# Kernel optimization log

Measured on AMD Instinct MI355X. Metric: run time of the kernel, lower is better.

Reference implementation:

```python
import jax, jax.numpy as jnp
import numpy as np

N, K, C = 2, 512, 256
IMG = 1024.0
P = 7            # output_size
S = 2            # sampling_ratio
SCALES = (0.25, 0.125, 0.0625, 0.03125)
MIN_LEVEL, MAX_LEVEL = 2, 5
CANON_SIZE, CANON_LEVEL = 224.0, 4


def setup_inputs() -> dict:
    key = jax.random.key(0)
    ks = jax.random.split(key, 7)
    feats = {}
    for i, (hw, kk) in enumerate(zip((256, 128, 64, 32), ks[:4])):
        feats[f"feat{i + 2}"] = jax.random.normal(kk, (N, C, hw, hw), dtype=jnp.float32)
    # boxes: centers uniform in image, sizes log-uniform in [32, 512] px -> spans all levels
    cxy = jax.random.uniform(ks[4], (N, K, 2), minval=0.0, maxval=IMG)
    wh = 32.0 * jnp.exp2(jax.random.uniform(ks[5], (N, K, 2), minval=0.0, maxval=4.0))
    x1y1 = jnp.clip(cxy - wh / 2, 0.0, IMG)
    x2y2 = jnp.clip(cxy + wh / 2, 0.0, IMG)
    boxes = jnp.concatenate([x1y1, x2y2], axis=-1).astype(jnp.float32)  # [N,K,4] xyxy
    feats["boxes"] = boxes
    return feats


def _roi_align_level(feat, boxes, batch_idx, scale):
    """ROIAlignV2 (aligned=True). feat [N,C,H,W], boxes [M,4] xyxy in image coords."""
    Nf, Cf, H, W = feat.shape
    M = boxes.shape[0]
    b = boxes * scale - 0.5  # aligned=True shift
    x1, y1, x2, y2 = b[:, 0], b[:, 1], b[:, 2], b[:, 3]
    bin_h = (y2 - y1) / P
    bin_w = (x2 - x1) / P
    # combined bin+sample grid: coord = start + ((i + 0.5)/S) * bin, i in [0, P*S)
    g = (jnp.arange(P * S, dtype=feat.dtype) + 0.5) / S  # [PS]
    y = y1[:, None] + g[None, :] * bin_h[:, None]  # [M, PS]
    x = x1[:, None] + g[None, :] * bin_w[:, None]  # [M, PS]

    def prep(c, size):
        valid = (c >= -1.0) & (c <= size)
        c = jnp.maximum(c, 0.0)
        lo = jnp.minimum(jnp.floor(c).astype(jnp.int32), size - 1)
        hi = jnp.minimum(lo + 1, size - 1)
        frac = c - lo.astype(c.dtype)  # harmless if >1 when lo==hi==size-1
        return lo, hi, frac, valid

    yl, yh, fy, vy = prep(y, H)
    xl, xh, fx, vx = prep(x, W)
    bi = batch_idx[:, None, None]

    def gather(yy, xx):
        # -> [M, PS, PS, C]
        return feat[bi, :, yy[:, :, None], xx[:, None, :]]

    fy_ = fy[:, :, None, None]
    fx_ = fx[:, None, :, None]
    v = ((1 - fy_) * ((1 - fx_) * gather(yl, xl) + fx_ * gather(yl, xh))
         + fy_ * ((1 - fx_) * gather(yh, xl) + fx_ * gather(yh, xh)))
    mask = (vy[:, :, None] & vx[:, None, :])[..., None]
    v = jnp.where(mask, v, jnp.zeros((), feat.dtype))
    out = v.reshape(M, P, S, P, S, Cf).mean(axis=(2, 4))  # avg over sampling grid
    return out.transpose(0, 3, 1, 2)  # [M, C, P, P]


def reference(feat2, feat3, feat4, feat5, boxes):
    feats = [feat2, feat3, feat4, feat5]
    flat = boxes.reshape(-1, 4)  # [M,4], concat over images
    batch_idx = jnp.repeat(jnp.arange(N, dtype=jnp.int32), K)
    # assign_boxes_to_levels
    area = (flat[:, 2] - flat[:, 0]) * (flat[:, 3] - flat[:, 1])
    sizes = jnp.sqrt(area)
    lvl = jnp.floor(CANON_LEVEL + jnp.log2(sizes / CANON_SIZE + 1e-8))
    lvl = jnp.clip(lvl, MIN_LEVEL, MAX_LEVEL).astype(jnp.int32) - MIN_LEVEL  # [M] in 0..3
    out = jnp.zeros((flat.shape[0], C, P, P), dtype=feat2.dtype)
    for l, (feat, scale) in enumerate(zip(feats, SCALES)):
        o = _roi_align_level(feat, flat, batch_idx, scale)
        out = jnp.where((lvl == l)[:, None, None, None], o, out)
    return out
```

## Files before the change

### kernel.cpp

```cpp
#include <hip/hip_runtime.h>
#include <math.h>
#include <stdint.h>

#define NBATCH 2
#define KBOX   512
#define NBOX   (NBATCH*KBOX)
#define CCH    256
#define NBIN   49
#define NCH    8
#define BPB    (CCH/NCH)
#define COUT   (CCH*NBIN)
#define WCAP   1152
#define HDRN   8
#define TAPN   (24*NBIN)

typedef const uint32_t __attribute__((address_space(1)))* gas_u32p;
typedef uint32_t       __attribute__((address_space(3)))* las_u32p;

__global__ __launch_bounds__(64) void box_prep_kernel(
    const float* __restrict__ boxes, int* __restrict__ hdr, int* __restrict__ taps)
{
    const int m    = blockIdx.x;
    const int lane = threadIdx.x;

    const float x1 = boxes[m*4+0];
    const float y1 = boxes[m*4+1];
    const float x2 = boxes[m*4+2];
    const float y2 = boxes[m*4+3];

    const float area = (x2 - x1) * (y2 - y1);
    const float size = sqrtf(area);
    float lvlf = floorf(4.0f + log2f(size / 224.0f + 1e-8f));
    lvlf = fminf(fmaxf(lvlf, 2.0f), 5.0f);
    const int lvl = (int)lvlf - 2;

    const int   H     = 256 >> lvl;
    const float scale = 0.25f / (float)(1 << lvl);
    const float Hf    = (float)H;

    const float bx1 = x1 * scale - 0.5f;
    const float by1 = y1 * scale - 0.5f;
    const float bin_w = (x2 * scale - 0.5f - bx1) / 7.0f;
    const float bin_h = (y2 * scale - 0.5f - by1) / 7.0f;

    const float sx_min = bx1 + 0.25f * bin_w;
    const float sx_max = bx1 + 6.75f * bin_w;
    const float sy_min = by1 + 0.25f * bin_h;
    const float sy_max = by1 + 6.75f * bin_h;
    const int wx0 = min((int)floorf(fmaxf(sx_min, 0.0f)), H - 1);
    const int wy0 = min((int)floorf(fmaxf(sy_min, 0.0f)), H - 1);
    const int wx1 = min(min((int)floorf(fmaxf(sx_max, 0.0f)), H - 1) + 1, H - 1);
    const int wy1 = min(min((int)floorf(fmaxf(sy_max, 0.0f)), H - 1) + 1, H - 1);
    const int wspan = wx1 - wx0 + 1;
    const int hspan = wy1 - wy0 + 1;
    const int wsz   = wspan * hspan;

    if (lane < NBIN) {
        const int py = lane / 7;
        const int px = lane - py * 7;
        const int base = m * TAPN;
        float* tapf = (float*)taps;

        #pragma unroll
        for (int s = 0; s < 4; ++s) {
            const int iy = s >> 1;
            const int ix = s & 1;
            const float gy = ((float)(2*py + iy) + 0.5f) * 0.5f;
            const float gx = ((float)(2*px + ix) + 0.5f) * 0.5f;
            const float yy = by1 + gy * bin_h;
            const float xx = bx1 + gx * bin_w;

            const bool valid = (yy >= -1.0f) && (yy <= Hf) && (xx >= -1.0f) && (xx <= Hf);

            const float yc = fmaxf(yy, 0.0f);
            const float xc = fmaxf(xx, 0.0f);
            int yl = min((int)floorf(yc), H - 1);
            int xl = min((int)floorf(xc), H - 1);
            const int yh = min(yl + 1, H - 1);
            const int xh = min(xl + 1, H - 1);
            const float fy = yc - (float)yl;
            float fx = xc - (float)xl;
            if (xh == xl) fx = 0.0f;

            const float vm  = valid ? 0.25f : 0.0f;
            const float wyl = (1.0f - fy) * vm;
            const float wyh = fy * vm;

            const int xr = xl - wx0;
            const int o_lo = (yl - wy0) * wspan + xr;
            const int o_hi = (yh - wy0) * wspan + xr;

            taps[base + (2*s  )*NBIN + lane] = o_lo;
            taps[base + (2*s+1)*NBIN + lane] = o_hi;
            tapf[base + (8 + 2*s  )*NBIN + lane] = wyl * (1.0f - fx);
            tapf[base + (8 + 2*s+1)*NBIN + lane] = wyh * (1.0f - fx);
            tapf[base + (16 + 2*s  )*NBIN + lane] = wyl * fx;
            tapf[base + (16 + 2*s+1)*NBIN + lane] = wyh * fx;
        }
    }

    if (lane == 0) {
        int* h = hdr + m * HDRN;
        h[0] = lvl;
        h[1] = H;
        h[2] = H * H;
        h[3] = wy0 * H + wx0;
        h[4] = wspan;
        h[5] = wsz;
    }
}

__global__ __launch_bounds__(256, 4) void roi_align_kernel(
    const float* __restrict__ f2, const float* __restrict__ f3,
    const float* __restrict__ f4, const float* __restrict__ f5,
    const int* __restrict__ hdr, const int* __restrict__ taps,
    float* __restrict__ out)
{
    const int bid  = blockIdx.x;
    const int m    = bid >> 5;
    const int cg   = bid & 31;
    const int tid  = threadIdx.x;
    const int lane = tid & 63;
    const int wid  = tid >> 6;
    const int b    = m >> 9;

    __shared__ float win[NCH * WCAP];

    const int* h = hdr + m * HDRN;
    const int lvl   = h[0];
    const int H     = h[1];
    const int HH    = h[2];
    const int woff  = h[3];
    const int wspan = h[4];
    const int wsz   = h[5];

    const float* fptr = (lvl == 0) ? f2 : (lvl == 1) ? f3 : (lvl == 2) ? f4 : f5;
    const int c0 = cg * NCH;
    const float* src0 = fptr + ((size_t)(b * CCH + c0)) * HH + woff;

    for (int i = tid; i < wsz; i += 256) {
        const int r   = i / wspan;
        const int col = i - r * wspan;
        const float* sp = src0 + r * H + col;
        const int ldsbase = i & ~63;
        #pragma unroll
        for (int c = 0; c < NCH; ++c) {
            __builtin_amdgcn_global_load_lds(
                (gas_u32p)(const void*)(sp + (size_t)c * HH),
                (las_u32p)(void*)(&win[c * WCAP + ldsbase]),
                4, 0, 0);
        }
    }
    if (tid < NCH) win[tid * WCAP + wsz] = 0.0f;

    const int lidx = (lane < NBIN) ? lane : NBIN - 1;
    const int tb = m * TAPN;
    const float* tf = (const float*)taps;

    int   o8 [8];
    float wlo[8];
    float whi[8];
    #pragma unroll
    for (int j = 0; j < 8; ++j) o8 [j] = taps[tb + j*NBIN + lidx];
    #pragma unroll
    for (int j = 0; j < 8; ++j) wlo[j] = tf[tb + (8  + j)*NBIN + lidx];
    #pragma unroll
    for (int j = 0; j < 8; ++j) whi[j] = tf[tb + (16 + j)*NBIN + lidx];

    __syncthreads();

    const float* wa = win + (wid * 2    ) * WCAP;
    const float* wb = win + (wid * 2 + 1) * WCAP;

    float acc0 = 0.0f, acc1 = 0.0f;
    #pragma unroll
    for (int j = 0; j < 8; ++j) {
        const int oj = o8[j];
        const float a_lo = wa[oj], a_hi = wa[oj + 1];
        const float b_lo = wb[oj], b_hi = wb[oj + 1];
        acc0 += wlo[j] * a_lo + whi[j] * a_hi;
        acc1 += wlo[j] * b_lo + whi[j] * b_hi;
    }

    if (lane < NBIN) {
        float* outp = out + (size_t)m * COUT + (size_t)(c0 + wid * 2) * NBIN + lane;
        __builtin_nontemporal_store(acc0, outp);
        __builtin_nontemporal_store(acc1, outp + NBIN);
    }
}

extern "C" void kernel_launch(void* const* d_in, const int* in_sizes, int n_in,
                              void* d_out, int out_size, void* d_ws, size_t ws_size,
                              hipStream_t stream) {
    const float* f2    = (const float*)d_in[0];
    const float* f3    = (const float*)d_in[1];
    const float* f4    = (const float*)d_in[2];
    const float* f5    = (const float*)d_in[3];
    const float* boxes = (const float*)d_in[4];
    float* outp = (float*)d_out;

    int* hdr  = (int*)d_ws;
    int* taps = (int*)d_ws + NBOX * HDRN;

    box_prep_kernel<<<dim3(NBOX), dim3(64), 0, stream>>>(boxes, hdr, taps);
    roi_align_kernel<<<dim3(NBOX * BPB), dim3(256), 0, stream>>>(
        f2, f3, f4, f5, hdr, taps, outp);
}
```

Baseline: 112.7 us.

## Give each wavefront its own channel window and drop the block barrier

```diff
diff --git a/kernel.cpp b/kernel.cpp
--- a/kernel.cpp
+++ b/kernel.cpp
@@ -7,7 +7,7 @@
 #define NBOX   (NBATCH*KBOX)
 #define CCH    256
 #define NBIN   49
-#define NCH    8
+#define NCH    4
 #define BPB    (CCH/NCH)
 #define COUT   (CCH*NBIN)
 #define WCAP   1152
@@ -107,18 +107,19 @@
         h[3] = wy0 * H + wx0;
         h[4] = wspan;
         h[5] = wsz;
+        h[6] = __float_as_int(1.0f / (float)wspan);
     }
 }
 
-__global__ __launch_bounds__(256, 4) void roi_align_kernel(
+__global__ __launch_bounds__(256, 8) void roi_align_kernel(
     const float* __restrict__ f2, const float* __restrict__ f3,
     const float* __restrict__ f4, const float* __restrict__ f5,
     const int* __restrict__ hdr, const int* __restrict__ taps,
     float* __restrict__ out)
 {
     const int bid  = blockIdx.x;
-    const int m    = bid >> 5;
-    const int cg   = bid & 31;
+    const int m    = bid >> 6;
+    const int cg   = bid & 63;
     const int tid  = threadIdx.x;
     const int lane = tid & 63;
     const int wid  = tid >> 6;
@@ -127,31 +128,28 @@
     __shared__ float win[NCH * WCAP];
 
     const int* h = hdr + m * HDRN;
-    const int lvl   = h[0];
-    const int H     = h[1];
-    const int HH    = h[2];
-    const int woff  = h[3];
-    const int wspan = h[4];
-    const int wsz   = h[5];
+    const int   lvl   = h[0];
+    const int   H     = h[1];
+    const int   HH    = h[2];
+    const int   woff  = h[3];
+    const int   wspan = h[4];
+    const int   wsz   = h[5];
+    const float rw    = __int_as_float(h[6]);
 
     const float* fptr = (lvl == 0) ? f2 : (lvl == 1) ? f3 : (lvl == 2) ? f4 : f5;
-    const int c0 = cg * NCH;
-    const float* src0 = fptr + ((size_t)(b * CCH + c0)) * HH + woff;
-
-    for (int i = tid; i < wsz; i += 256) {
-        const int r   = i / wspan;
+    const int c = cg * NCH + wid;
+    const float* src0 = fptr + ((size_t)(b * CCH + c)) * HH + woff;
+    float* wbase = win + wid * WCAP;
+
+    for (int i = lane; i < wsz; i += 64) {
+        const int r   = (int)(((float)i + 0.5f) * rw);
         const int col = i - r * wspan;
-        const float* sp = src0 + r * H + col;
-        const int ldsbase = i & ~63;
-        #pragma unroll
-        for (int c = 0; c < NCH; ++c) {
-            __builtin_amdgcn_global_load_lds(
-                (gas_u32p)(const void*)(sp + (size_t)c * HH),
-                (las_u32p)(void*)(&win[c * WCAP + ldsbase]),
-                4, 0, 0);
-        }
-    }
-    if (tid < NCH) win[tid * WCAP + wsz] = 0.0f;
+        __builtin_amdgcn_global_load_lds(
+            (gas_u32p)(const void*)(src0 + r * H + col),
+            (las_u32p)(void*)(&wbase[i & ~63]),
+            4, 0, 0);
+    }
+    if (lane == 0) wbase[wsz] = 0.0f;
 
     const int lidx = (lane < NBIN) ? lane : NBIN - 1;
     const int tb = m * TAPN;
@@ -167,25 +165,19 @@
     #pragma unroll
     for (int j = 0; j < 8; ++j) whi[j] = tf[tb + (16 + j)*NBIN + lidx];
 
-    __syncthreads();
-
-    const float* wa = win + (wid * 2    ) * WCAP;
-    const float* wb = win + (wid * 2 + 1) * WCAP;
-
-    float acc0 = 0.0f, acc1 = 0.0f;
+    asm volatile("s_waitcnt vmcnt(0) lgkmcnt(0)" ::: "memory");
+    __builtin_amdgcn_sched_barrier(0);
+
+    float acc = 0.0f;
     #pragma unroll
     for (int j = 0; j < 8; ++j) {
         const int oj = o8[j];
-        const float a_lo = wa[oj], a_hi = wa[oj + 1];
-        const float b_lo = wb[oj], b_hi = wb[oj + 1];
-        acc0 += wlo[j] * a_lo + whi[j] * a_hi;
-        acc1 += wlo[j] * b_lo + whi[j] * b_hi;
+        acc += wlo[j] * wbase[oj] + whi[j] * wbase[oj + 1];
     }
 
     if (lane < NBIN) {
-        float* outp = out + (size_t)m * COUT + (size_t)(c0 + wid * 2) * NBIN + lane;
-        __builtin_nontemporal_store(acc0, outp);
-        __builtin_nontemporal_store(acc1, outp + NBIN);
+        __builtin_nontemporal_store(
+            acc, out + (size_t)m * COUT + (size_t)c * NBIN + lane);
     }
 }
 
```

Result: slower. 117.4 us (+4.2%).
